# Kernel optimization log

Measured on AMD Instinct MI355X. Metric: run time of the kernel, lower is better.

The kernel has to match this reference:

```python
import jax, jax.numpy as jnp
import numpy as np

INPUT_SIZE = 512   # num_embeddings == RNN input feature dim
SEQ = INPUT_SIZE // 4   # 128, embedding dim == RNN seq_len
HID = 12
OUT = 3
B = 2048


def setup_inputs() -> dict:
    key = jax.random.key(0)
    ks = jax.random.split(key, 12)
    s = 0.1
    x = jax.random.randint(ks[0], (B, INPUT_SIZE), 0, INPUT_SIZE)
    emb = jax.random.normal(ks[1], (INPUT_SIZE, SEQ), dtype=jnp.float32) * s
    w_ih_f = jax.random.normal(ks[2], (HID, INPUT_SIZE), dtype=jnp.float32) * s
    w_hh_f = jax.random.normal(ks[3], (HID, HID), dtype=jnp.float32) * s
    b_ih_f = jax.random.normal(ks[4], (HID,), dtype=jnp.float32) * s
    b_hh_f = jax.random.normal(ks[5], (HID,), dtype=jnp.float32) * s
    w_ih_r = jax.random.normal(ks[6], (HID, INPUT_SIZE), dtype=jnp.float32) * s
    w_hh_r = jax.random.normal(ks[7], (HID, HID), dtype=jnp.float32) * s
    b_ih_r = jax.random.normal(ks[8], (HID,), dtype=jnp.float32) * s
    b_hh_r = jax.random.normal(ks[9], (HID,), dtype=jnp.float32) * s
    fc_w = jax.random.normal(ks[10], (OUT, 2 * HID), dtype=jnp.float32) * s
    fc_b = jax.random.normal(ks[11], (OUT,), dtype=jnp.float32) * s
    return {"x": x, "emb": emb,
            "w_ih_f": w_ih_f, "w_hh_f": w_hh_f, "b_ih_f": b_ih_f, "b_hh_f": b_hh_f,
            "w_ih_r": w_ih_r, "w_hh_r": w_hh_r, "b_ih_r": b_ih_r, "b_hh_r": b_hh_r,
            "fc_w": fc_w, "fc_b": fc_b}


def reference(x, emb, w_ih_f, w_hh_f, b_ih_f, b_hh_f,
              w_ih_r, w_hh_r, b_ih_r, b_hh_r, fc_w, fc_b):
    # embedding lookup: (B, INPUT_SIZE) -> (B, INPUT_SIZE, SEQ)
    e = emb[x]
    # view(-1, input_size, seq) is a no-op on this contiguous shape; swapaxes(1,2)
    xs = jnp.swapaxes(e, 1, 2)  # (B, SEQ, INPUT_SIZE): seq_len=SEQ, feat=INPUT_SIZE

    # forward-direction tanh RNN: precompute input projections, scan the recurrence
    pre = jnp.einsum('bsi,hi->sbh', xs, w_ih_f) + b_ih_f  # (SEQ, B, HID)

    def step(h, p):
        h = jnp.tanh(p + h @ w_hh_f.T + b_hh_f)
        return h, None

    h0 = jnp.zeros((xs.shape[0], HID), dtype=xs.dtype)
    h_fwd, _ = jax.lax.scan(step, h0, pre)  # final forward hidden (B, HID)

    # reverse-direction output at the LAST timestep = one step from zero hidden
    # on x_{T-1} (only out[:, -1, :] is consumed by the module)
    h_bwd = jnp.tanh(xs[:, -1, :] @ w_ih_r.T + b_ih_r + b_hh_r)  # (B, HID)

    out_last = jnp.concatenate([h_fwd, h_bwd], axis=-1)  # (B, 2*HID)
    return out_last @ fc_w.T + fc_b  # (B, OUT)
```

## Files before the change

### kernel.cpp

```cpp
#include <hip/hip_runtime.h>
#include <hip/hip_bf16.h>

#define B_N     2048
#define IN_N    512
#define SEQ_N   128
#define HID_N   12
#define HP_N    16
#define OUT_N   3

typedef __attribute__((ext_vector_type(8))) short short8;
typedef __attribute__((ext_vector_type(4))) float f32x4;
typedef unsigned int uint;
typedef unsigned short ushort;

__device__ __forceinline__ float fast_tanh(float x) {
    float e = __builtin_amdgcn_exp2f(x * 2.8853900817779268f);
    return 1.0f - 2.0f * __builtin_amdgcn_rcpf(e + 1.0f);
}

__device__ __forceinline__ ushort f2bf(float f) {
    uint u = __float_as_uint(f);
    u += 0x7fffu + ((u >> 16) & 1u);
    return (ushort)(u >> 16);
}

__device__ __forceinline__ float bf2f(ushort s) {
    return __uint_as_float(((uint)s) << 16);
}

__global__ __launch_bounds__(256) void k_prep(
    const float* __restrict__ emb, const float* __restrict__ w_ih_f,
    ushort* __restrict__ embB, ushort* __restrict__ wBT)
{
    int tid = blockIdx.x * 256 + threadIdx.x;
    float4 e = ((const float4*)emb)[tid];
    uint2 o;
    o.x = (uint)f2bf(e.x) | ((uint)f2bf(e.y) << 16);
    o.y = (uint)f2bf(e.z) | ((uint)f2bf(e.w) << 16);
    ((uint2*)embB)[tid] = o;
    if (tid < 16 * IN_N)
        wBT[tid] = (tid < HID_N * IN_N) ? f2bf(w_ih_f[tid]) : (ushort)0;
}

__global__ __launch_bounds__(256, 4) void k_pre(
    const int* __restrict__ x, const ushort* __restrict__ embB,
    const ushort* __restrict__ wBT, ushort* __restrict__ preB)
{
    __shared__ int xb[IN_N];
    __shared__ __align__(16) ushort As[128 * 136];

    const int t = threadIdx.x;
    const int b = blockIdx.x;

    ((int2*)xb)[t] = ((const int2*)(x + b * IN_N))[t];
    __syncthreads();

    const int l      = t & 63;
    const int w      = t >> 6;
    const int lane16 = l & 15;
    const int quad   = l >> 4;
    const int il     = w * 32 + quad * 8;

    f32x4 acc[2] = {{0.f,0.f,0.f,0.f},{0.f,0.f,0.f,0.f}};

    uint R[8][4];

    #pragma unroll
    for (int j = 0; j < 8; ++j) {
        const uint4 v = *(const uint4*)(embB + (size_t)xb[il + j] * SEQ_N + lane16 * 8);
        R[j][0] = v.x; R[j][1] = v.y; R[j][2] = v.z; R[j][3] = v.w;
    }

    for (int c = 0; c < 4; ++c) {
        short8 bfr[4];
        #pragma unroll
        for (int ks = 0; ks < 4; ++ks)
            bfr[ks] = *(const short8*)(wBT + lane16 * IN_N + c * 128 + ks * 32 + quad * 8);

        if (c) __syncthreads();

        #pragma unroll
        for (int p = 0; p < 8; ++p) {
            const uint sel = (p & 1) ? 0x07060302u : 0x05040100u;
            const int pv = p >> 1;
            uint u0 = __builtin_amdgcn_perm(R[1][pv], R[0][pv], sel);
            uint u1 = __builtin_amdgcn_perm(R[3][pv], R[2][pv], sel);
            uint u2 = __builtin_amdgcn_perm(R[5][pv], R[4][pv], sel);
            uint u3 = __builtin_amdgcn_perm(R[7][pv], R[6][pv], sel);
            *(uint4*)&As[(size_t)(lane16 * 8 + p) * 136 + il] =
                make_uint4(u0, u1, u2, u3);
        }

        if (c < 3) {
            const int ibase = (c + 1) * 128 + il;
            #pragma unroll
            for (int j = 0; j < 8; ++j) {
                const uint4 v = *(const uint4*)(embB + (size_t)xb[ibase + j] * SEQ_N + lane16 * 8);
                R[j][0] = v.x; R[j][1] = v.y; R[j][2] = v.z; R[j][3] = v.w;
            }
        }
        __syncthreads();

        #pragma unroll
        for (int tt = 0; tt < 2; ++tt) {
            const int row = (w * 2 + tt) * 16 + lane16;
            #pragma unroll
            for (int ks = 0; ks < 4; ++ks) {
                short8 af = *(const short8*)&As[row * 136 + ks * 32 + quad * 8];
                acc[tt] = __builtin_amdgcn_mfma_f32_16x16x32_bf16(af, bfr[ks], acc[tt], 0, 0, 0);
            }
        }
    }

    if (lane16 < HID_N) {
        #pragma unroll
        for (int tt = 0; tt < 2; ++tt) {
            #pragma unroll
            for (int r = 0; r < 4; ++r) {
                int s = (w * 2 + tt) * 16 + quad * 4 + r;
                preB[((size_t)b * SEQ_N + s) * HP_N + lane16] = f2bf(acc[tt][r]);
            }
        }
    }
}

__global__ __launch_bounds__(256) void k_rev(
    const int* __restrict__ x, const float* __restrict__ emb,
    const float* __restrict__ w_ih_r,
    const float* __restrict__ b_ih_r, const float* __restrict__ b_hh_r,
    float* __restrict__ rev)
{
    const int b = blockIdx.x * 4 + (threadIdx.x >> 6);
    const int l = threadIdx.x & 63;

    float p[12];
    #pragma unroll
    for (int h = 0; h < 12; ++h) p[h] = 0.f;

    for (int k = 0; k < 8; ++k) {
        int i = l + k * 64;
        int r = x[b * IN_N + i];
        float ev = emb[r * SEQ_N + 127];
        #pragma unroll
        for (int h = 0; h < 12; ++h) p[h] += ev * w_ih_r[h * IN_N + i];
    }
    #pragma unroll
    for (int off = 32; off; off >>= 1) {
        #pragma unroll
        for (int h = 0; h < 12; ++h) p[h] += __shfl_xor(p[h], off);
    }
    if (l == 0) {
        #pragma unroll
        for (int h = 0; h < 12; ++h)
            rev[b * HP_N + h] = fast_tanh(p[h] + b_ih_r[h] + b_hh_r[h]);
        #pragma unroll
        for (int h = 12; h < 16; ++h) rev[b * HP_N + h] = 0.f;
    }
}

__global__ __launch_bounds__(256) void k_rnn(
    const ushort* __restrict__ preB, const float* __restrict__ rev,
    const float* __restrict__ w_hh_f,
    const float* __restrict__ b_ih_f, const float* __restrict__ b_hh_f,
    const float* __restrict__ fc_w, const float* __restrict__ fc_b,
    float* __restrict__ out)
{
    __shared__ float ho[16][40];

    const int tid = threadIdx.x;
    const int l   = tid & 63;
    const int j   = l & 15;
    const int jj  = (j < 12) ? j : 0;
    const int gid = tid >> 4;
    const int b   = blockIdx.x * 16 + gid;
    const int baseaddr = (l & 48) << 2;

    const float4* wr = (const float4*)(w_hh_f + jj * 12);
    float4 w0 = wr[0], w1 = wr[1], w2 = wr[2];
    float W[12] = {w0.x, w0.y, w0.z, w0.w, w1.x, w1.y, w1.z, w1.w,
                   w2.x, w2.y, w2.z, w2.w};
    const float bias = b_ih_f[jj] + b_hh_f[jj];

    const ushort* pb = preB + (size_t)b * SEQ_N * HP_N + j;
    ushort pq[8];
    #pragma unroll
    for (int k = 0; k < 8; ++k) pq[k] = pb[k * HP_N];

    float h = 0.f;
    for (int s8 = 0; s8 < 16; ++s8) {
        #pragma unroll
        for (int k = 0; k < 8; ++k) {
            int s = s8 * 8 + k;
            float p = bf2f(pq[k]) + bias;
            pq[k] = pb[((s + 8) & 127) * HP_N];
            int hb = __float_as_int(h);
            float hk[12];
            #pragma unroll
            for (int kk = 0; kk < 12; ++kk)
                hk[kk] = __int_as_float(__builtin_amdgcn_ds_bpermute(baseaddr + 4 * kk, hb));
            float c0 = p, c1 = 0.f, c2 = 0.f;
            #pragma unroll
            for (int u = 0; u < 4; ++u) {
                c0 = __builtin_fmaf(W[u],     hk[u],     c0);
                c1 = __builtin_fmaf(W[4 + u], hk[4 + u], c1);
                c2 = __builtin_fmaf(W[8 + u], hk[8 + u], c2);
            }
            h = fast_tanh(c0 + c1 + c2);
        }
    }

    ho[gid][j]      = h;
    ho[gid][20 + j] = rev[b * HP_N + j];
    if (j < OUT_N) {
        const float* fw = fc_w + j * 24;
        float o = fc_b[j];
        #pragma unroll
        for (int k = 0; k < 12; ++k)
            o += fw[k] * ho[gid][k] + fw[12 + k] * ho[gid][20 + k];
        out[b * OUT_N + j] = o;
    }
}

extern "C" void kernel_launch(void* const* d_in, const int* in_sizes, int n_in,
                              void* d_out, int out_size, void* d_ws, size_t ws_size,
                              hipStream_t stream) {
    const int*   x      = (const int*)  d_in[0];
    const float* emb    = (const float*)d_in[1];
    const float* w_ih_f = (const float*)d_in[2];
    const float* w_hh_f = (const float*)d_in[3];
    const float* b_ih_f = (const float*)d_in[4];
    const float* b_hh_f = (const float*)d_in[5];
    const float* w_ih_r = (const float*)d_in[6];
    const float* b_ih_r = (const float*)d_in[8];
    const float* b_hh_r = (const float*)d_in[9];
    const float* fc_w   = (const float*)d_in[10];
    const float* fc_b   = (const float*)d_in[11];
    float* out = (float*)d_out;

    ushort* preB = (ushort*)d_ws;
    float*  rev  = (float*)((char*)d_ws + 8388608);
    ushort* embB = (ushort*)((char*)d_ws + 8519680);
    ushort* wBT  = (ushort*)((char*)d_ws + 8650752);

    k_prep<<<64,   256, 0, stream>>>(emb, w_ih_f, embB, wBT);
    k_pre <<<B_N,  256, 0, stream>>>(x, embB, wBT, preB);
    k_rev <<<B_N/4,256, 0, stream>>>(x, emb, w_ih_r, b_ih_r, b_hh_r, rev);
    k_rnn <<<B_N/16,256,0, stream>>>(preB, rev, w_hh_f, b_ih_f, b_hh_f, fc_w, fc_b, out);
}
```

Before: 143.6 us.

## Fuse reverse-direction projection into MFMA pre-projection kernel with XOR-swizzled LDS

Removes the separate k_rev kernel and computes the reverse-direction input projection as an extra MFMA accumulator inside k_pre. It reuses the already-staged A tile for the last timestep rows, with w_ih_r converted to bf16 in the prep kernel. The LDS tile drops its padding in favour of an XOR swizzle to avoid bank conflicts, and the launch bound changes occupancy from 4 to 2. This saves a kernel launch and the redundant gather of embedding data, but the reverse path now runs in bf16 instead of fp32 and register pressure goes up.

```diff
diff --git a/kernel.cpp b/kernel.cpp
--- a/kernel.cpp
+++ b/kernel.cpp
@@ -30,7 +30,8 @@
 
 __global__ __launch_bounds__(256) void k_prep(
     const float* __restrict__ emb, const float* __restrict__ w_ih_f,
-    ushort* __restrict__ embB, ushort* __restrict__ wBT)
+    const float* __restrict__ w_ih_r,
+    ushort* __restrict__ embB, ushort* __restrict__ wBT, ushort* __restrict__ wRT)
 {
     int tid = blockIdx.x * 256 + threadIdx.x;
     float4 e = ((const float4*)emb)[tid];
@@ -38,16 +39,21 @@
     o.x = (uint)f2bf(e.x) | ((uint)f2bf(e.y) << 16);
     o.y = (uint)f2bf(e.z) | ((uint)f2bf(e.w) << 16);
     ((uint2*)embB)[tid] = o;
-    if (tid < 16 * IN_N)
-        wBT[tid] = (tid < HID_N * IN_N) ? f2bf(w_ih_f[tid]) : (ushort)0;
-}
-
-__global__ __launch_bounds__(256, 4) void k_pre(
+    if (tid < 16 * IN_N) {
+        bool live = tid < HID_N * IN_N;
+        wBT[tid] = live ? f2bf(w_ih_f[tid]) : (ushort)0;
+        wRT[tid] = live ? f2bf(w_ih_r[tid]) : (ushort)0;
+    }
+}
+
+__global__ __launch_bounds__(256, 2) void k_pre(
     const int* __restrict__ x, const ushort* __restrict__ embB,
-    const ushort* __restrict__ wBT, ushort* __restrict__ preB)
+    const ushort* __restrict__ wBT, const ushort* __restrict__ wRT,
+    const float* __restrict__ b_ih_r, const float* __restrict__ b_hh_r,
+    ushort* __restrict__ preB, float* __restrict__ rev)
 {
     __shared__ int xb[IN_N];
-    __shared__ __align__(16) ushort As[128 * 136];
+    __shared__ __align__(16) ushort As[128 * 128];
 
     const int t = threadIdx.x;
     const int b = blockIdx.x;
@@ -60,8 +66,11 @@
     const int lane16 = l & 15;
     const int quad   = l >> 4;
     const int il     = w * 32 + quad * 8;
+    const int wg     = w * 4 + quad;
+    const int wsx    = lane16 & 7;
 
     f32x4 acc[2] = {{0.f,0.f,0.f,0.f},{0.f,0.f,0.f,0.f}};
+    f32x4 accR   = {0.f,0.f,0.f,0.f};
 
     uint R[8][4];
 
@@ -72,10 +81,12 @@
     }
 
     for (int c = 0; c < 4; ++c) {
-        short8 bfr[4];
-        #pragma unroll
-        for (int ks = 0; ks < 4; ++ks)
-            bfr[ks] = *(const short8*)(wBT + lane16 * IN_N + c * 128 + ks * 32 + quad * 8);
+        short8 bfr[4], bfrR[4];
+        #pragma unroll
+        for (int ks = 0; ks < 4; ++ks) {
+            bfr[ks]  = *(const short8*)(wBT + lane16 * IN_N + c * 128 + ks * 32 + quad * 8);
+            bfrR[ks] = *(const short8*)(wRT + lane16 * IN_N + c * 128 + ks * 32 + quad * 8);
+        }
 
         if (c) __syncthreads();
 
@@ -87,7 +98,8 @@
             uint u1 = __builtin_amdgcn_perm(R[3][pv], R[2][pv], sel);
             uint u2 = __builtin_amdgcn_perm(R[5][pv], R[4][pv], sel);
             uint u3 = __builtin_amdgcn_perm(R[7][pv], R[6][pv], sel);
-            *(uint4*)&As[(size_t)(lane16 * 8 + p) * 136 + il] =
+            const int s = lane16 * 8 + p;
+            *(uint4*)&As[(size_t)s * 128 + (size_t)(wg ^ wsx) * 8] =
                 make_uint4(u0, u1, u2, u3);
         }
 
@@ -104,10 +116,14 @@
         #pragma unroll
         for (int tt = 0; tt < 2; ++tt) {
             const int row = (w * 2 + tt) * 16 + lane16;
+            const int rsx = (row >> 3) & 7;
             #pragma unroll
             for (int ks = 0; ks < 4; ++ks) {
-                short8 af = *(const short8*)&As[row * 136 + ks * 32 + quad * 8];
+                short8 af = *(const short8*)&As[(size_t)row * 128 +
+                                                (size_t)(((ks * 4 + quad) ^ rsx)) * 8];
                 acc[tt] = __builtin_amdgcn_mfma_f32_16x16x32_bf16(af, bfr[ks], acc[tt], 0, 0, 0);
+                if (tt == 1)
+                    accR = __builtin_amdgcn_mfma_f32_16x16x32_bf16(af, bfrR[ks], accR, 0, 0, 0);
             }
         }
     }
@@ -121,40 +137,9 @@
                 preB[((size_t)b * SEQ_N + s) * HP_N + lane16] = f2bf(acc[tt][r]);
             }
         }
-    }
-}
-
-__global__ __launch_bounds__(256) void k_rev(
-    const int* __restrict__ x, const float* __restrict__ emb,
-    const float* __restrict__ w_ih_r,
-    const float* __restrict__ b_ih_r, const float* __restrict__ b_hh_r,
-    float* __restrict__ rev)
-{
-    const int b = blockIdx.x * 4 + (threadIdx.x >> 6);
-    const int l = threadIdx.x & 63;
-
-    float p[12];
-    #pragma unroll
-    for (int h = 0; h < 12; ++h) p[h] = 0.f;
-
-    for (int k = 0; k < 8; ++k) {
-        int i = l + k * 64;
-        int r = x[b * IN_N + i];
-        float ev = emb[r * SEQ_N + 127];
-        #pragma unroll
-        for (int h = 0; h < 12; ++h) p[h] += ev * w_ih_r[h * IN_N + i];
-    }
-    #pragma unroll
-    for (int off = 32; off; off >>= 1) {
-        #pragma unroll
-        for (int h = 0; h < 12; ++h) p[h] += __shfl_xor(p[h], off);
-    }
-    if (l == 0) {
-        #pragma unroll
-        for (int h = 0; h < 12; ++h)
-            rev[b * HP_N + h] = fast_tanh(p[h] + b_ih_r[h] + b_hh_r[h]);
-        #pragma unroll
-        for (int h = 12; h < 16; ++h) rev[b * HP_N + h] = 0.f;
+        if (w == 3 && quad == 3)
+            rev[b * HP_N + lane16] =
+                fast_tanh(accR[3] + b_ih_r[lane16] + b_hh_r[lane16]);
     }
 }
 
@@ -241,9 +226,9 @@
     float*  rev  = (float*)((char*)d_ws + 8388608);
     ushort* embB = (ushort*)((char*)d_ws + 8519680);
     ushort* wBT  = (ushort*)((char*)d_ws + 8650752);
-
-    k_prep<<<64,   256, 0, stream>>>(emb, w_ih_f, embB, wBT);
-    k_pre <<<B_N,  256, 0, stream>>>(x, embB, wBT, preB);
-    k_rev <<<B_N/4,256, 0, stream>>>(x, emb, w_ih_r, b_ih_r, b_hh_r, rev);
+    ushort* wRT  = (ushort*)((char*)d_ws + 8667136);
+
+    k_prep<<<64,   256, 0, stream>>>(emb, w_ih_f, w_ih_r, embB, wBT, wRT);
+    k_pre <<<B_N,  256, 0, stream>>>(x, embB, wBT, wRT, b_ih_r, b_hh_r, preB, rev);
     k_rnn <<<B_N/16,256,0, stream>>>(preB, rev, w_hh_f, b_ih_f, b_hh_f, fc_w, fc_b, out);
 }
```

New measurement: 138.2 us. 3.7% less time.
